# Kernel tuning notes

Measured on AMD Instinct MI355X. Metric: run time of the kernel, lower is better.

## Reference

```python
import jax, jax.numpy as jnp
import numpy as np

B, HW, N_L = 8, 5476, 32
DIM, L_IN, KC, VC, NH = 1024, 768, 1024, 1024, 8
EPS = 1e-5


def conv1(w, b, x):
    # 1x1 Conv1d == per-position linear. x: [B, C_in, L] -> [B, C_out, L]
    return jnp.einsum('oc,bcl->bol', w, x) + b[None, :, None]


def inorm(y):
    # InstanceNorm1d (affine=False): normalize each (batch, channel) over length.
    m = jnp.mean(y, axis=-1, keepdims=True)
    v = jnp.var(y, axis=-1, keepdims=True)
    return (y - m) * jax.lax.rsqrt(v + EPS)


def setup_inputs() -> dict:
    key = jax.random.key(0)
    ks = jax.random.split(key, 10)
    s = 0.02  # weight init scale
    x = jax.random.normal(ks[0], (B, HW, DIM), jnp.float32)
    l = jax.random.normal(ks[1], (B, N_L, L_IN), jnp.float32)
    l_mask = jax.random.randint(ks[2], (B, N_L, 1), 0, 2).astype(jnp.float32)
    l_mask = l_mask.at[:, 0, :].set(1.0)  # ensure at least one valid token
    return {
        'x': x, 'l': l, 'l_mask': l_mask,
        'vis_w': jax.random.normal(ks[3], (DIM, DIM), jnp.float32) * s,
        'vis_b': jnp.zeros((DIM,), jnp.float32),
        'fq_w': jax.random.normal(ks[4], (KC, DIM), jnp.float32) * s,
        'fq_b': jnp.zeros((KC,), jnp.float32),
        'fk_w': jax.random.normal(ks[5], (KC, L_IN), jnp.float32) * s,
        'fk_b': jnp.zeros((KC,), jnp.float32),
        'fv_w': jax.random.normal(ks[6], (VC, L_IN), jnp.float32) * s,
        'fv_b': jnp.zeros((VC,), jnp.float32),
        'W_w': jax.random.normal(ks[7], (VC, VC), jnp.float32) * s,
        'W_b': jnp.zeros((VC,), jnp.float32),
        'pm_w': jax.random.normal(ks[8], (VC, VC), jnp.float32) * s,
        'pm_b': jnp.zeros((VC,), jnp.float32),
    }


def reference(x, l, l_mask, vis_w, vis_b, fq_w, fq_b, fk_w, fk_b,
              fv_w, fv_b, W_w, W_b, pm_w, pm_b):
    # PWAM forward (eval mode, dropout=0)
    b, hw, _ = x.shape
    n_l = l.shape[1]
    xt = jnp.transpose(x, (0, 2, 1))            # [B, dim, HW]
    lt = jnp.transpose(l, (0, 2, 1))            # [B, l_in, N_l]
    mt = jnp.transpose(l_mask, (0, 2, 1))       # [B, 1, N_l]

    # vis_project: conv1d + GELU
    vis = jax.nn.gelu(conv1(vis_w, vis_b, xt), approximate=False)  # [B, dim, HW]

    # SpatialImageLanguageAttention
    q = inorm(conv1(fq_w, fq_b, xt))            # [B, KC, HW]
    k = conv1(fk_w, fk_b, lt) * mt              # [B, KC, N_l]
    v = conv1(fv_w, fv_b, lt) * mt              # [B, VC, N_l]

    qh = q.reshape(b, NH, KC // NH, hw).transpose(0, 1, 3, 2)  # [B, H, HW, dk]
    kh = k.reshape(b, NH, KC // NH, n_l)                       # [B, H, dk, N_l]
    vh = v.reshape(b, NH, VC // NH, n_l)                       # [B, H, dv, N_l]

    sim = jnp.einsum('bhqd,bhdk->bhqk', qh, kh) * (KC ** -0.5)
    sim = sim + (10000.0 * mt[:, None] - 10000.0)              # masked bias
    sim = jax.nn.softmax(sim, axis=-1)                          # [B, H, HW, N_l]

    out = jnp.einsum('bhqk,bhdk->bhqd', sim, vh)                # [B, H, HW, dv]
    out = out.transpose(0, 2, 1, 3).reshape(b, hw, VC)          # [B, HW, VC]
    out = jnp.transpose(out, (0, 2, 1))                         # [B, VC, HW]
    lang = inorm(conv1(W_w, W_b, out))                          # [B, VC, HW]

    # gated fusion + project_mm
    mm = vis * lang
    mm = jax.nn.gelu(conv1(pm_w, pm_b, mm), approximate=False)
    return jnp.transpose(mm, (0, 2, 1))                         # [B, HW, VC]
```

## Files before the change

### kernel.cpp

```cpp
#include <hip/hip_runtime.h>

typedef _Float16 f16;
typedef _Float16 f16x4 __attribute__((ext_vector_type(4)));
typedef _Float16 f16x8 __attribute__((ext_vector_type(8)));
typedef float f32x4 __attribute__((ext_vector_type(4)));

#define NB   8
#define HW   5476
#define NL   32
#define DIM  1024
#define LIN  768
#define MTOT (NB * HW)
#define MT256 ((MTOT + 255) / 256)
#define CSPLIT 128


__device__ __forceinline__ void g2l16(const void* g, void* l) {
#if __has_builtin(__builtin_amdgcn_global_load_lds)
  __builtin_amdgcn_global_load_lds(
      (const __attribute__((address_space(1))) void*)g,
      (__attribute__((address_space(3))) void*)l, 16, 0, 0);
#else
  const int lane = threadIdx.x & 63;
  *(uint4*)((char*)l + lane * 16) = *(const uint4*)g;
#endif
}

__device__ __forceinline__ float gelu_f(float x) {
  return 0.5f * x * (1.0f + erff(x * 0.70710678118654752f));
}

template <int EPI, int EPI2>
__global__ __launch_bounds__(512, 2) void gemm256(
    const f16* __restrict__ A, const f16* __restrict__ W,
    const float* __restrict__ bias, void* __restrict__ out,
    const f16* __restrict__ W2, const float* __restrict__ bias2,
    void* __restrict__ out2, int M) {
  constexpr int K = 1024, N = 1024;
  constexpr int NT = (EPI2 >= 0) ? 8 : 4;
  constexpr int NWG = NT * MT256;
  constexpr int CHUNK = NWG / 8;
  __shared__ f16 lds[2][2][256 * 64];

  const int L = blockIdx.x;
  const int w = (L & 7) * CHUNK + (L >> 3);
  const int mt = w / NT;
  int nt = w % NT;
  const f16* Wp = W;
  const float* bp = bias;
  void* op = out;
  bool second = false;
  if constexpr (EPI2 >= 0) {
    if (nt >= 4) {
      nt -= 4;
      Wp = W2;
      bp = bias2;
      op = out2;
      second = true;
    }
  }

  const int tid = threadIdx.x;
  const int wave = tid >> 6, lane = tid & 63;
  const int m0 = mt * 256, n0 = nt * 256;
  const int wm = (wave >> 2) * 128;
  const int wn = (wave & 3) * 64;
  const int fr = lane & 15, fq = lane >> 4;

  f32x4 acc[8][4];
#pragma unroll
  for (int i = 0; i < 8; ++i)
#pragma unroll
    for (int j = 0; j < 4; ++j) acc[i][j] = (f32x4){0.f, 0.f, 0.f, 0.f};

  const int sub = lane >> 3;
  const int scol = ((lane & 7) ^ sub) * 8;

  const f16* Abase = A + (size_t)0;

  auto stage = [&](int buf, int k0) {
#pragma unroll
    for (int i = 0; i < 4; ++i) {
      const int r = wave * 32 + i * 8;
      int gm = m0 + r + sub;
      if (gm > M - 1) gm = M - 1;
      g2l16(Abase + (size_t)gm * K + k0 + scol, &lds[buf][0][r * 64]);
    }
#pragma unroll
    for (int i = 0; i < 4; ++i) {
      const int r = wave * 32 + i * 8;
      g2l16(Wp + (size_t)(n0 + r + sub) * K + k0 + scol, &lds[buf][1][r * 64]);
    }
  };

  stage(0, 0);
  for (int it = 0; it < K / 64; ++it) {
    const int cur = it & 1;
    if (it < K / 64 - 1) {
      stage(cur ^ 1, (it + 1) * 64);
      asm volatile("s_waitcnt vmcnt(8)" ::: "memory");
    } else {
      asm volatile("s_waitcnt vmcnt(0)" ::: "memory");
    }
    asm volatile("s_barrier" ::: "memory");

#pragma unroll
    for (int ks = 0; ks < 2; ++ks) {
      const int ko = ks * 32 + fq * 8;
      const int kos = ko ^ ((fr & 7) << 3);
      f16x8 af[8], bf[4];
#pragma unroll
      for (int i = 0; i < 8; ++i)
        af[i] = *(const f16x8*)&lds[cur][0][(wm + i * 16 + fr) * 64 + kos];
#pragma unroll
      for (int j = 0; j < 4; ++j)
        bf[j] = *(const f16x8*)&lds[cur][1][(wn + j * 16 + fr) * 64 + kos];
#pragma unroll
      for (int i = 0; i < 8; ++i)
#pragma unroll
        for (int j = 0; j < 4; ++j)
          acc[i][j] = __builtin_amdgcn_mfma_f32_16x16x32_f16(af[i], bf[j],
                                                             acc[i][j], 0, 0, 0);
    }
    asm volatile("s_waitcnt lgkmcnt(0)" ::: "memory");
    asm volatile("s_barrier" ::: "memory");
  }

  const bool do_gelu = second ? (EPI2 == 0 || EPI2 == 3) : (EPI == 0 || EPI == 3);
  const bool to_f16 = second ? (EPI2 <= 1) : (EPI <= 1);
  const int row0 = m0 + wm + fq * 4;
  const int col0 = n0 + wn + fr;
#pragma unroll
  for (int j = 0; j < 4; ++j) {
    const int col = col0 + j * 16;
    const float bv = bp[col];
#pragma unroll
    for (int i = 0; i < 8; ++i) {
#pragma unroll
      for (int r = 0; r < 4; ++r) {
        const int row = row0 + i * 16 + r;
        if (row < M) {
          float v = acc[i][j][r] + bv;
          if (do_gelu) v = gelu_f(v);
          if (to_f16)
            ((f16*)op)[(size_t)row * N + col] = (f16)v;
          else
            ((float*)op)[(size_t)row * N + col] = v;
        }
      }
    }
  }
}

__global__ void cvt_f32_f16(const float* __restrict__ in, f16* __restrict__ out,
                            int nchunks) {
  const int i = blockIdx.x * 256 + threadIdx.x;
  if (i >= nchunks) return;
  const float4* p = (const float4*)in + (size_t)i * 2;
  const float4 a = p[0], b = p[1];
  f16x8 o = {(f16)a.x, (f16)a.y, (f16)a.z, (f16)a.w,
             (f16)b.x, (f16)b.y, (f16)b.z, (f16)b.w};
  *((f16x8*)out + i) = o;
}

template <typename T>
__global__ __launch_bounds__(256) void colstats_partial(
    const T* __restrict__ X, float* __restrict__ psum,
    float* __restrict__ psq) {
  const int b = blockIdx.y;
  const int sp = blockIdx.x;
  const int c = threadIdx.x * 4;
  constexpr int CHUNK = (HW + CSPLIT - 1) / CSPLIT;
  const int r0 = sp * CHUNK;
  const int r1 = (r0 + CHUNK < HW) ? r0 + CHUNK : HW;

  float s0 = 0.f, s1 = 0.f, s2 = 0.f, s3 = 0.f;
  float q0 = 0.f, q1 = 0.f, q2 = 0.f, q3 = 0.f;
  const T* base = X + ((size_t)b * HW + r0) * DIM + c;
  for (int r = r0; r < r1; ++r) {
    float v0, v1, v2, v3;
    if constexpr (sizeof(T) == 2) {
      const f16x4 v = *(const f16x4*)base;
      v0 = (float)v[0]; v1 = (float)v[1]; v2 = (float)v[2]; v3 = (float)v[3];
    } else {
      const float4 v = *(const float4*)base;
      v0 = v.x; v1 = v.y; v2 = v.z; v3 = v.w;
    }
    s0 += v0; s1 += v1; s2 += v2; s3 += v3;
    q0 += v0 * v0; q1 += v1 * v1; q2 += v2 * v2; q3 += v3 * v3;
    base += DIM;
  }
  const size_t o = ((size_t)sp * NB + b) * DIM + c;
  *(float4*)&psum[o] = make_float4(s0, s1, s2, s3);
  *(float4*)&psq[o] = make_float4(q0, q1, q2, q3);
}

__global__ __launch_bounds__(256) void colstats_final(
    const float* __restrict__ psum, const float* __restrict__ psq,
    float* __restrict__ mean, float* __restrict__ rinv) {
  const int i = blockIdx.x * 256 + threadIdx.x;
  float s = 0.f, q = 0.f;
  for (int sp = 0; sp < CSPLIT; ++sp) {
    s += psum[(size_t)sp * NB * DIM + i];
    q += psq[(size_t)sp * NB * DIM + i];
  }
  const float m = s * (1.0f / HW);
  const float var = q * (1.0f / HW) - m * m;
  mean[i] = m;
  rinv[i] = rsqrtf(var + 1e-5f);
}

__global__ __launch_bounds__(256) void kv_gemm(
    const float* __restrict__ l, const float* __restrict__ lmask,
    const float* __restrict__ wk, const float* __restrict__ bk,
    const float* __restrict__ wv, const float* __restrict__ bv,
    float* __restrict__ Kout, float* __restrict__ Vout) {
  const int b = blockIdx.z;
  const int o0 = blockIdx.x * 64;
  const float* w = blockIdx.y ? wv : wk;
  const float* bb = blockIdx.y ? bv : bk;
  float* out = blockIdx.y ? Vout : Kout;

  __shared__ float wl[64 * 129];
  __shared__ float ll[32 * 129];
  const int tid = threadIdx.x;
  const int o = tid & 63, ng = tid >> 6;
  float acc[8];
#pragma unroll
  for (int j = 0; j < 8; ++j) acc[j] = 0.f;

  for (int kc = 0; kc < LIN; kc += 128) {
    for (int e = tid; e < 64 * 128; e += 256)
      wl[(e >> 7) * 129 + (e & 127)] =
          w[(size_t)(o0 + (e >> 7)) * LIN + kc + (e & 127)];
    for (int e = tid; e < 32 * 128; e += 256)
      ll[(e >> 7) * 129 + (e & 127)] =
          l[(size_t)b * NL * LIN + (size_t)(e >> 7) * LIN + kc + (e & 127)];
    __syncthreads();
    for (int k = 0; k < 128; ++k) {
      const float wv_ = wl[o * 129 + k];
#pragma unroll
      for (int j = 0; j < 8; ++j) acc[j] += wv_ * ll[(ng * 8 + j) * 129 + k];
    }
    __syncthreads();
  }
  const float bval = bb[o0 + o];
#pragma unroll
  for (int j = 0; j < 8; ++j) {
    const int n = ng * 8 + j;
    out[((size_t)b * DIM + o0 + o) * NL + n] =
        (acc[j] + bval) * lmask[b * NL + n];
  }
}

__global__ __launch_bounds__(256) void attn_kernel(
    const f16* __restrict__ Q, const float* __restrict__ qmean,
    const float* __restrict__ qrinv, const float* __restrict__ Kk,
    const float* __restrict__ Vv, const float* __restrict__ lmask,
    float* __restrict__ Out) {
  const int b = blockIdx.z, h = blockIdx.y;
  __shared__ float ks[128 * NL], vs[128 * NL], qm[128], qr[128], bs[NL];
  const int tid = threadIdx.x;
  const float* kbase = Kk + ((size_t)b * DIM + h * 128) * NL;
  const float* vbase = Vv + ((size_t)b * DIM + h * 128) * NL;
  for (int i = tid; i < 128 * NL; i += 256) {
    ks[i] = kbase[i];
    vs[i] = vbase[i];
  }
  if (tid < 128) {
    qm[tid] = qmean[b * DIM + h * 128 + tid];
    qr[tid] = qrinv[b * DIM + h * 128 + tid];
  }
  if (tid < NL) bs[tid] = (lmask[b * NL + tid] - 1.0f) * 10000.0f;
  __syncthreads();

  const int mloc = blockIdx.x * 256 + tid;
  if (mloc >= HW) return;
  const size_t m = (size_t)b * HW + mloc;
  const f16* qrow = Q + m * DIM + h * 128;

  float sc[32];
#pragma unroll
  for (int n = 0; n < 32; ++n) sc[n] = 0.f;

  for (int d8 = 0; d8 < 16; ++d8) {
    const f16x8 qv = *(const f16x8*)(qrow + d8 * 8);
#pragma unroll
    for (int j = 0; j < 8; ++j) {
      const int d = d8 * 8 + j;
      const float qd = ((float)qv[j] - qm[d]) * qr[d];
      const float4* kr = (const float4*)&ks[d * 32];
#pragma unroll
      for (int n4 = 0; n4 < 8; ++n4) {
        const float4 kk = kr[n4];
        sc[n4 * 4 + 0] += qd * kk.x;
        sc[n4 * 4 + 1] += qd * kk.y;
        sc[n4 * 4 + 2] += qd * kk.z;
        sc[n4 * 4 + 3] += qd * kk.w;
      }
    }
  }
  float mx = -1e30f;
#pragma unroll
  for (int n = 0; n < 32; ++n) {
    sc[n] = sc[n] * 0.03125f + bs[n];
    mx = fmaxf(mx, sc[n]);
  }
  float sum = 0.f;
#pragma unroll
  for (int n = 0; n < 32; ++n) {
    sc[n] = __expf(sc[n] - mx);
    sum += sc[n];
  }
  const float rs = 1.0f / sum;

  float* orow = Out + m * DIM + h * 128;
  for (int dv8 = 0; dv8 < 16; ++dv8) {
    float ov[8];
#pragma unroll
    for (int j = 0; j < 8; ++j) {
      const float4* vr = (const float4*)&vs[(dv8 * 8 + j) * 32];
      float a = 0.f;
#pragma unroll
      for (int n4 = 0; n4 < 8; ++n4) {
        const float4 vv = vr[n4];
        a += sc[n4 * 4 + 0] * vv.x + sc[n4 * 4 + 1] * vv.y +
             sc[n4 * 4 + 2] * vv.z + sc[n4 * 4 + 3] * vv.w;
      }
      ov[j] = a * rs;
    }
    float4* op = (float4*)(orow + dv8 * 8);
    op[0] = make_float4(ov[0], ov[1], ov[2], ov[3]);
    op[1] = make_float4(ov[4], ov[5], ov[6], ov[7]);
  }
}

__global__ void center_kernel(const float* __restrict__ X,
                              const float* __restrict__ mean,
                              f16* __restrict__ out, int nchunks) {
  const int i = blockIdx.x * 256 + threadIdx.x;
  if (i >= nchunks) return;
  const size_t e = (size_t)i * 8;
  const int mrow = (int)(e >> 10);
  const int o = (int)(e & 1023);
  const int b = mrow / HW;
  const float4* p = (const float4*)(X + e);
  const float4 a = p[0], c = p[1];
  const float* mn = mean + b * DIM + o;
  f16x8 r = {(f16)(a.x - mn[0]), (f16)(a.y - mn[1]), (f16)(a.z - mn[2]),
             (f16)(a.w - mn[3]), (f16)(c.x - mn[4]), (f16)(c.y - mn[5]),
             (f16)(c.z - mn[6]), (f16)(c.w - mn[7])};
  *((f16x8*)out + i) = r;
}

__global__ void fuse_kernel(const f16* __restrict__ vis,
                            const float* __restrict__ lang,
                            const float* __restrict__ mean,
                            const float* __restrict__ rinv,
                            f16* __restrict__ out, int nchunks) {
  const int i = blockIdx.x * 256 + threadIdx.x;
  if (i >= nchunks) return;
  const size_t e = (size_t)i * 8;
  const int mrow = (int)(e >> 10);
  const int o = (int)(e & 1023);
  const int b = mrow / HW;
  const f16x8 v = *((const f16x8*)vis + i);
  const float4* p = (const float4*)(lang + e);
  const float4 a = p[0], c = p[1];
  const float lv[8] = {a.x, a.y, a.z, a.w, c.x, c.y, c.z, c.w};
  const float* mn = mean + b * DIM + o;
  const float* ri = rinv + b * DIM + o;
  f16x8 r;
#pragma unroll
  for (int j = 0; j < 8; ++j)
    r[j] = (f16)((float)v[j] * ((lv[j] - mn[j]) * ri[j]));
  *((f16x8*)out + i) = r;
}

extern "C" void kernel_launch(void* const* d_in, const int* in_sizes, int n_in,
                              void* d_out, int out_size, void* d_ws,
                              size_t ws_size, hipStream_t stream) {
  const float* x     = (const float*)d_in[0];
  const float* l     = (const float*)d_in[1];
  const float* lmask = (const float*)d_in[2];
  const float* vis_w = (const float*)d_in[3];
  const float* vis_b = (const float*)d_in[4];
  const float* fq_w  = (const float*)d_in[5];
  const float* fq_b  = (const float*)d_in[6];
  const float* fk_w  = (const float*)d_in[7];
  const float* fk_b  = (const float*)d_in[8];
  const float* fv_w  = (const float*)d_in[9];
  const float* fv_b  = (const float*)d_in[10];
  const float* W_w   = (const float*)d_in[11];
  const float* W_b   = (const float*)d_in[12];
  const float* pm_w  = (const float*)d_in[13];
  const float* pm_b  = (const float*)d_in[14];

  char* ws = (char*)d_ws;
  const size_t SB = (size_t)MTOT * DIM * 2;
  f16* Ah = (f16*)(ws);
  f16* Bh = (f16*)(ws + SB);
  f16* Ch = (f16*)(ws + 2 * SB);
  float* Df = (float*)(ws + 3 * SB);
  char* wsp = ws + 5 * SB;
  f16* vis_wh = (f16*)(wsp);
  f16* fq_wh  = (f16*)(wsp + (1 << 21));
  f16* W_wh   = (f16*)(wsp + 2 * (1 << 21));
  f16* pm_wh  = (f16*)(wsp + 3 * (1 << 21));
  float* Kout = (float*)(wsp + 4 * (1 << 21));
  float* Vout = (float*)(wsp + 4 * (1 << 21) + (1 << 20));
  float* st   = (float*)(wsp + 4 * (1 << 21) + 2 * (1 << 20));
  float* qmean = st;
  float* qrinv = st + 8192;
  float* amean = st + 16384;
  float* arinv = st + 24576;
  float* lmean = st + 32768;
  float* lrinv = st + 40960;
  float* psum  = (float*)(wsp + 4 * (1 << 21) + 3 * (1 << 20));
  float* psq   = psum + (size_t)CSPLIT * NB * DIM;

  const int NCH_BIG = MTOT * DIM / 8;
  const int NCH_W = DIM * DIM / 8;

  cvt_f32_f16<<<(NCH_BIG + 255) / 256, 256, 0, stream>>>(x, Ah, NCH_BIG);
  cvt_f32_f16<<<(NCH_W + 255) / 256, 256, 0, stream>>>(vis_w, vis_wh, NCH_W);
  cvt_f32_f16<<<(NCH_W + 255) / 256, 256, 0, stream>>>(fq_w, fq_wh, NCH_W);
  cvt_f32_f16<<<(NCH_W + 255) / 256, 256, 0, stream>>>(W_w, W_wh, NCH_W);
  cvt_f32_f16<<<(NCH_W + 255) / 256, 256, 0, stream>>>(pm_w, pm_wh, NCH_W);

  kv_gemm<<<dim3(16, 2, 8), 256, 0, stream>>>(l, lmask, fk_w, fk_b, fv_w, fv_b,
                                              Kout, Vout);

  gemm256<0, 1><<<8 * MT256, 512, 0, stream>>>(
      Ah, vis_wh, vis_b, Bh, fq_wh, fq_b, Ch, MTOT);

  colstats_partial<f16><<<dim3(CSPLIT, NB), 256, 0, stream>>>(Ch, psum, psq);
  colstats_final<<<32, 256, 0, stream>>>(psum, psq, qmean, qrinv);

  attn_kernel<<<dim3((HW + 255) / 256, 8, 8), 256, 0, stream>>>(
      Ch, qmean, qrinv, Kout, Vout, lmask, Df);

  colstats_partial<float><<<dim3(CSPLIT, NB), 256, 0, stream>>>(Df, psum, psq);
  colstats_final<<<32, 256, 0, stream>>>(psum, psq, amean, arinv);
  center_kernel<<<(NCH_BIG + 255) / 256, 256, 0, stream>>>(Df, amean, Ah,
                                                           NCH_BIG);

  gemm256<2, -1><<<4 * MT256, 512, 0, stream>>>(
      Ah, W_wh, W_b, Df, nullptr, nullptr, nullptr, MTOT);
  colstats_partial<float><<<dim3(CSPLIT, NB), 256, 0, stream>>>(Df, psum, psq);
  colstats_final<<<32, 256, 0, stream>>>(psum, psq, lmean, lrinv);
  fuse_kernel<<<(NCH_BIG + 255) / 256, 256, 0, stream>>>(Bh, Df, lmean, lrinv,
                                                         Ah, NCH_BIG);

  gemm256<3, -1><<<4 * MT256, 512, 0, stream>>>(
      Ah, pm_wh, pm_b, d_out, nullptr, nullptr, nullptr, MTOT);
}
```

Before: 1.449 ms.

## Deepen GEMM LDS pipeline to four 32-wide K stages with prefetch distance three

Replaces the double-buffered 64-wide K loop with a four-buffer ring of 32-wide K tiles, issuing loads three stages ahead so that only one barrier is needed per step. It adds a new XOR swizzle layout for the 32-wide tiles and raises wave priority around the MFMA block. The goal is to hide global-to-LDS latency better and to drop the second barrier per iteration. The cost is twice as many loop iterations and tighter vmcnt accounting.

```diff
diff --git a/kernel.cpp b/kernel.cpp
--- a/kernel.cpp
+++ b/kernel.cpp
@@ -30,6 +30,17 @@
   return 0.5f * x * (1.0f + erff(x * 0.70710678118654752f));
 }
 
+#define WAITV(N) asm volatile("s_waitcnt vmcnt(" #N ")" ::: "memory")
+__device__ __forceinline__ void barrier_nf() {
+  asm volatile("s_barrier" ::: "memory");
+}
+
+__device__ __forceinline__ int swz32(int r, int q) {
+  const int p = r >> 1;
+  const int c = (((r & 1) << 2) | q) ^ (p & 7);
+  return p * 64 + c * 8;
+}
+
 template <int EPI, int EPI2>
 __global__ __launch_bounds__(512, 2) void gemm256(
     const f16* __restrict__ A, const f16* __restrict__ W,
@@ -37,10 +48,11 @@
     const f16* __restrict__ W2, const float* __restrict__ bias2,
     void* __restrict__ out2, int M) {
   constexpr int K = 1024, N = 1024;
+  constexpr int KT = K / 32;
   constexpr int NT = (EPI2 >= 0) ? 8 : 4;
   constexpr int NWG = NT * MT256;
   constexpr int CHUNK = NWG / 8;
-  __shared__ f16 lds[2][2][256 * 64];
+  __shared__ f16 lds[4][2][256 * 32];
 
   const int L = blockIdx.x;
   const int w = (L & 7) * CHUNK + (L >> 3);
@@ -73,58 +85,65 @@
 #pragma unroll
     for (int j = 0; j < 4; ++j) acc[i][j] = (f32x4){0.f, 0.f, 0.f, 0.f};
 
-  const int sub = lane >> 3;
-  const int scol = ((lane & 7) ^ sub) * 8;
-
-  const f16* Abase = A + (size_t)0;
-
-  auto stage = [&](int buf, int k0) {
-#pragma unroll
-    for (int i = 0; i < 4; ++i) {
-      const int r = wave * 32 + i * 8;
-      int gm = m0 + r + sub;
+  const int plocal = lane >> 3;
+  const int csw = (lane & 7) ^ plocal;
+  const int rofs = plocal * 2 + (csw >> 2);
+  const int qofs = (csw & 3) * 8;
+
+  auto stage = [&](int t) {
+    const int buf = t & 3;
+    const int k0 = t * 32;
+    f16* Ab = &lds[buf][0][0];
+    f16* Bb = &lds[buf][1][0];
+#pragma unroll
+    for (int la = 0; la < 2; ++la) {
+      const int rg = wave * 2 + la;
+      int gm = m0 + rg * 16 + rofs;
       if (gm > M - 1) gm = M - 1;
-      g2l16(Abase + (size_t)gm * K + k0 + scol, &lds[buf][0][r * 64]);
-    }
-#pragma unroll
-    for (int i = 0; i < 4; ++i) {
-      const int r = wave * 32 + i * 8;
-      g2l16(Wp + (size_t)(n0 + r + sub) * K + k0 + scol, &lds[buf][1][r * 64]);
+      g2l16(A + (size_t)gm * K + k0 + qofs, &Ab[rg * 512]);
+    }
+#pragma unroll
+    for (int la = 0; la < 2; ++la) {
+      const int rg = wave * 2 + la;
+      const int gn = n0 + rg * 16 + rofs;
+      g2l16(Wp + (size_t)gn * K + k0 + qofs, &Bb[rg * 512]);
     }
   };
 
-  stage(0, 0);
-  for (int it = 0; it < K / 64; ++it) {
-    const int cur = it & 1;
-    if (it < K / 64 - 1) {
-      stage(cur ^ 1, (it + 1) * 64);
-      asm volatile("s_waitcnt vmcnt(8)" ::: "memory");
-    } else {
-      asm volatile("s_waitcnt vmcnt(0)" ::: "memory");
-    }
-    asm volatile("s_barrier" ::: "memory");
-
-#pragma unroll
-    for (int ks = 0; ks < 2; ++ks) {
-      const int ko = ks * 32 + fq * 8;
-      const int kos = ko ^ ((fr & 7) << 3);
-      f16x8 af[8], bf[4];
-#pragma unroll
-      for (int i = 0; i < 8; ++i)
-        af[i] = *(const f16x8*)&lds[cur][0][(wm + i * 16 + fr) * 64 + kos];
+  auto compute = [&](int t) {
+    const f16* Ab = &lds[t & 3][0][0];
+    const f16* Bb = &lds[t & 3][1][0];
+    f16x8 af[8], bf[4];
+#pragma unroll
+    for (int i = 0; i < 8; ++i)
+      af[i] = *(const f16x8*)&Ab[swz32(wm + i * 16 + fr, fq)];
+#pragma unroll
+    for (int j = 0; j < 4; ++j)
+      bf[j] = *(const f16x8*)&Bb[swz32(wn + j * 16 + fr, fq)];
+    __builtin_amdgcn_s_setprio(1);
+#pragma unroll
+    for (int i = 0; i < 8; ++i)
 #pragma unroll
       for (int j = 0; j < 4; ++j)
-        bf[j] = *(const f16x8*)&lds[cur][1][(wn + j * 16 + fr) * 64 + kos];
-#pragma unroll
-      for (int i = 0; i < 8; ++i)
-#pragma unroll
-        for (int j = 0; j < 4; ++j)
-          acc[i][j] = __builtin_amdgcn_mfma_f32_16x16x32_f16(af[i], bf[j],
-                                                             acc[i][j], 0, 0, 0);
-    }
-    asm volatile("s_waitcnt lgkmcnt(0)" ::: "memory");
-    asm volatile("s_barrier" ::: "memory");
-  }
+        acc[i][j] = __builtin_amdgcn_mfma_f32_16x16x32_f16(af[i], bf[j],
+                                                           acc[i][j], 0, 0, 0);
+    __builtin_amdgcn_s_setprio(0);
+  };
+
+  stage(0);
+  stage(1);
+  stage(2);
+#pragma unroll 4
+  for (int t = 0; t < KT - 4; ++t) {
+    WAITV(8);
+    barrier_nf();
+    stage(t + 3);
+    compute(t);
+  }
+  WAITV(8); barrier_nf(); stage(KT - 1); compute(KT - 4);
+  WAITV(8); barrier_nf(); compute(KT - 3);
+  WAITV(4); barrier_nf(); compute(KT - 2);
+  WAITV(0); barrier_nf(); compute(KT - 1);
 
   const bool do_gelu = second ? (EPI2 == 0 || EPI2 == 3) : (EPI == 0 || EPI == 3);
   const bool to_f16 = second ? (EPI2 <= 1) : (EPI <= 1);
```

After: 1.439 ms. No clear change (-0.7%).

## Interleave split global-to-LDS staging with MFMA phases in GEMM main loop

Applied to the files above, without the earlier changes.

Restructures the 256x256 GEMM K-loop into four phases per K-tile. Each phase interleaves LDS fragment reads, half-tile prefetch of the next A/B tiles, and a 16-MFMA cluster with raised wave priority, so that global loads overlap compute more finely. It also changes tile rasterization to walk M fastest within each N column, aiming for better L2 reuse of the weight tile. The extra barriers per tile add synchronization cost, and the whole-tile vmcnt(0) wait before the last phase may stall.

```diff
diff --git a/kernel.cpp b/kernel.cpp
--- a/kernel.cpp
+++ b/kernel.cpp
@@ -30,6 +30,11 @@
   return 0.5f * x * (1.0f + erff(x * 0.70710678118654752f));
 }
 
+#define WAITV(N) asm volatile("s_waitcnt vmcnt(" #N ")" ::: "memory")
+__device__ __forceinline__ void barrier_nf() {
+  asm volatile("s_barrier" ::: "memory");
+}
+
 template <int EPI, int EPI2>
 __global__ __launch_bounds__(512, 2) void gemm256(
     const f16* __restrict__ A, const f16* __restrict__ W,
@@ -37,6 +42,7 @@
     const f16* __restrict__ W2, const float* __restrict__ bias2,
     void* __restrict__ out2, int M) {
   constexpr int K = 1024, N = 1024;
+  constexpr int KT = K / 64;
   constexpr int NT = (EPI2 >= 0) ? 8 : 4;
   constexpr int NWG = NT * MT256;
   constexpr int CHUNK = NWG / 8;
@@ -44,8 +50,8 @@
 
   const int L = blockIdx.x;
   const int w = (L & 7) * CHUNK + (L >> 3);
-  const int mt = w / NT;
-  int nt = w % NT;
+  const int mt = w % MT256;
+  int nt = w / MT256;
   const f16* Wp = W;
   const float* bp = bias;
   void* op = out;
@@ -73,57 +79,88 @@
 #pragma unroll
     for (int j = 0; j < 4; ++j) acc[i][j] = (f32x4){0.f, 0.f, 0.f, 0.f};
 
-  const int sub = lane >> 3;
-  const int scol = ((lane & 7) ^ sub) * 8;
-
-  const f16* Abase = A + (size_t)0;
-
-  auto stage = [&](int buf, int k0) {
+  const int sub8 = lane >> 3;
+  const int srcc = ((lane & 7) ^ sub8) * 8;
+
+  auto stageA = [&](int t, int half) {
+    const int buf = t & 1, k0 = t * 64;
+#pragma unroll
+    for (int k = 0; k < 2; ++k) {
+      const int rl = (wave * 2 + k) * 8 + sub8;
+      int gm = m0 + half * 128 + rl;
+      if (gm > M - 1) gm = M - 1;
+      g2l16(A + (size_t)gm * K + k0 + srcc,
+            &lds[buf][0][half * 8192 + (wave * 2 + k) * 512]);
+    }
+  };
+  auto stageB = [&](int t, int half) {
+    const int buf = t & 1, k0 = t * 64;
+#pragma unroll
+    for (int k = 0; k < 2; ++k) {
+      const int rl = (wave * 2 + k) * 8 + sub8;
+      const int gn = n0 + half * 128 + rl;
+      g2l16(Wp + (size_t)gn * K + k0 + srcc,
+            &lds[buf][1][half * 8192 + (wave * 2 + k) * 512]);
+    }
+  };
+
+  f16x8 bf[4];
+  auto readB = [&](int t, int s) {
+    const f16* Bb = &lds[t & 1][1][0];
+#pragma unroll
+    for (int j = 0; j < 4; ++j) {
+      const int row = wn + j * 16 + fr;
+      bf[j] = *(const f16x8*)&Bb[row * 64 + (((s * 4 + fq) ^ (row & 7)) * 8)];
+    }
+  };
+  auto readA = [&](int t, int q, int s, f16x8* af) {
+    const f16* Ab = &lds[t & 1][0][0];
 #pragma unroll
     for (int i = 0; i < 4; ++i) {
-      const int r = wave * 32 + i * 8;
-      int gm = m0 + r + sub;
-      if (gm > M - 1) gm = M - 1;
-      g2l16(Abase + (size_t)gm * K + k0 + scol, &lds[buf][0][r * 64]);
-    }
-#pragma unroll
-    for (int i = 0; i < 4; ++i) {
-      const int r = wave * 32 + i * 8;
-      g2l16(Wp + (size_t)(n0 + r + sub) * K + k0 + scol, &lds[buf][1][r * 64]);
+      const int row = wm + (q * 4 + i) * 16 + fr;
+      af[i] = *(const f16x8*)&Ab[row * 64 + (((s * 4 + fq) ^ (row & 7)) * 8)];
     }
   };
-
-  stage(0, 0);
-  for (int it = 0; it < K / 64; ++it) {
-    const int cur = it & 1;
-    if (it < K / 64 - 1) {
-      stage(cur ^ 1, (it + 1) * 64);
-      asm volatile("s_waitcnt vmcnt(8)" ::: "memory");
-    } else {
-      asm volatile("s_waitcnt vmcnt(0)" ::: "memory");
-    }
-    asm volatile("s_barrier" ::: "memory");
-
-#pragma unroll
-    for (int ks = 0; ks < 2; ++ks) {
-      const int ko = ks * 32 + fq * 8;
-      const int kos = ko ^ ((fr & 7) << 3);
-      f16x8 af[8], bf[4];
-#pragma unroll
-      for (int i = 0; i < 8; ++i)
-        af[i] = *(const f16x8*)&lds[cur][0][(wm + i * 16 + fr) * 64 + kos];
+  auto mfma16 = [&](int q, const f16x8* af) {
+    __builtin_amdgcn_s_setprio(1);
+#pragma unroll
+    for (int i = 0; i < 4; ++i)
 #pragma unroll
       for (int j = 0; j < 4; ++j)
-        bf[j] = *(const f16x8*)&lds[cur][1][(wn + j * 16 + fr) * 64 + kos];
-#pragma unroll
-      for (int i = 0; i < 8; ++i)
-#pragma unroll
-        for (int j = 0; j < 4; ++j)
-          acc[i][j] = __builtin_amdgcn_mfma_f32_16x16x32_f16(af[i], bf[j],
-                                                             acc[i][j], 0, 0, 0);
-    }
-    asm volatile("s_waitcnt lgkmcnt(0)" ::: "memory");
-    asm volatile("s_barrier" ::: "memory");
+        acc[q * 4 + i][j] = __builtin_amdgcn_mfma_f32_16x16x32_f16(
+            af[i], bf[j], acc[q * 4 + i][j], 0, 0, 0);
+    __builtin_amdgcn_s_setprio(0);
+  };
+
+  stageA(0, 0); stageB(0, 0); stageA(0, 1); stageB(0, 1);
+  WAITV(0);
+  barrier_nf();
+
+  for (int t = 0; t < KT; ++t) {
+    f16x8 af[4];
+    const bool pf = (t + 1 < KT);
+    readB(t, 0);
+    readA(t, 0, 0, af);
+    if (pf) { stageA(t + 1, 0); stageB(t + 1, 0); }
+    barrier_nf();
+    mfma16(0, af);
+    barrier_nf();
+    readA(t, 1, 0, af);
+    if (pf) stageA(t + 1, 1);
+    barrier_nf();
+    mfma16(1, af);
+    barrier_nf();
+    readB(t, 1);
+    readA(t, 0, 1, af);
+    if (pf) stageB(t + 1, 1);
+    barrier_nf();
+    mfma16(0, af);
+    barrier_nf();
+    readA(t, 1, 1, af);
+    WAITV(0);
+    barrier_nf();
+    mfma16(1, af);
+    barrier_nf();
   }
 
   const bool do_gelu = second ? (EPI2 == 0 || EPI2 == 3) : (EPI == 0 || EPI == 3);
```

After: 1.482 ms. 2.3% more time.
